# Kernel tuning notes

Hardware: AMD Instinct MI355X
Metric: run time of the kernel (lower is better)

## Reference

```python
import jax, jax.numpy as jnp
import numpy as np

N, E, H, L = 50000, 1_600_000, 128, 3


def _ln(x, g, b, eps=1e-5):
    m = x.mean(-1, keepdims=True)
    v = x.var(-1, keepdims=True)
    return (x - m) / jnp.sqrt(v + eps) * g + b


def _mlp2(inp, w1, b1, g, be, w2, b2):
    # Linear -> LayerNorm -> SiLU -> (Dropout=identity in eval) -> Linear
    h = inp @ w1 + b1
    h = jax.nn.silu(_ln(h, g, be))
    return h @ w2 + b2


def setup_inputs() -> dict:
    key = jax.random.key(0)
    ks = jax.random.split(key, 16)
    s = 0.05
    inp = {
        'x': jax.random.normal(ks[0], (N, 7), jnp.float32),
        'pos': jax.random.normal(ks[1], (N, 3), jnp.float32),
        'edge_index': jax.random.randint(ks[2], (2, E), 0, N, jnp.int64),
        'enc_w1': jax.random.normal(ks[3], (7, H)) * s,
        'enc_b1': jnp.zeros((H,)),
        'enc_g': jnp.ones((H,)),
        'enc_be': jnp.zeros((H,)),
        'enc_w2': jax.random.normal(ks[4], (H, H)) * s,
        'enc_b2': jnp.zeros((H,)),
        'e_w1': jax.random.normal(ks[5], (L, 2 * H + 5, H)) * s,
        'e_b1': jnp.zeros((L, H)),
        'e_g': jnp.ones((L, H)),
        'e_be': jnp.zeros((L, H)),
        'e_w2': jax.random.normal(ks[6], (L, H, H)) * s,
        'e_b2': jnp.zeros((L, H)),
        'n_w1': jax.random.normal(ks[7], (L, 2 * H, H)) * s,
        'n_b1': jnp.zeros((L, H)),
        'n_g': jnp.ones((L, H)),
        'n_be': jnp.zeros((L, H)),
        'n_w2': jax.random.normal(ks[8], (L, H, H)) * s,
        'n_b2': jnp.zeros((L, H)),
        'ln_g': jnp.ones((L, H)),
        'ln_b': jnp.zeros((L, H)),
        'dec_w1': jax.random.normal(ks[9], (H, H)) * s,
        'dec_b1': jnp.zeros((H,)),
        'dec_w2': jax.random.normal(ks[10], (H, H // 2)) * s,
        'dec_b2': jnp.zeros((H // 2,)),
        'dec_w3': jax.random.normal(ks[11], (H // 2, 6)) * s,
        'dec_b3': jnp.zeros((6,)),
    }
    return inp


def reference(x, pos, edge_index, enc_w1, enc_b1, enc_g, enc_be, enc_w2, enc_b2,
              e_w1, e_b1, e_g, e_be, e_w2, e_b2,
              n_w1, n_b1, n_g, n_be, n_w2, n_b2,
              ln_g, ln_b, dec_w1, dec_b1, dec_w2, dec_b2, dec_w3, dec_b3):
    n_nodes = x.shape[0]
    row, col = edge_index[0], edge_index[1]  # row=source(j), col=target(i)

    # physics edge features: [dist, direction(3), 1/r^2]
    diff = pos[col] - pos[row]                          # (E,3)
    dist = jnp.linalg.norm(diff, axis=-1, keepdims=True) + 1e-8
    edge_attr = jnp.concatenate([dist, diff / dist, 1.0 / (dist ** 2 + 1e-6)], -1)

    h = _mlp2(x, enc_w1, enc_b1, enc_g, enc_be, enc_w2, enc_b2)  # (N,H)

    for l in range(L):
        # message: cat(x_i, x_j, edge_attr) -> edge MLP
        msg_in = jnp.concatenate([h[col], h[row], edge_attr], -1)  # (E,2H+5)
        msg = _mlp2(msg_in, e_w1[l], e_b1[l], e_g[l], e_be[l], e_w2[l], e_b2[l])
        # scatter-add aggregate to targets
        aggr = jax.ops.segment_sum(msg, col, num_segments=n_nodes)  # (N,H)
        # update: cat(x, aggr) -> node MLP, then residual + LayerNorm
        h_new = _mlp2(jnp.concatenate([h, aggr], -1),
                      n_w1[l], n_b1[l], n_g[l], n_be[l], n_w2[l], n_b2[l])
        h = _ln(h + h_new, ln_g[l], ln_b[l])

    d = jax.nn.silu(h @ dec_w1 + dec_b1)
    d = jax.nn.silu(d @ dec_w2 + dec_b2)
    delta = d @ dec_w3 + dec_b3                                  # (N,6)
    return x[:, :6] + delta
```

## Files before the change

### kernel.cpp

```cpp
#include <hip/hip_runtime.h>

typedef unsigned short u16;
typedef unsigned int u32;
typedef __bf16 bf16x8 __attribute__((ext_vector_type(8)));
typedef float f32x4 __attribute__((ext_vector_type(4)));
typedef float f32x2 __attribute__((ext_vector_type(2)));

#define AS_STRIDE 136

__device__ __forceinline__ u16 f2bf1(float f) {
  union { __bf16 h; u16 u; } c; c.h = (__bf16)f; return c.u;
}
__device__ __forceinline__ u32 cvt2bf(float a, float b) {
  union { __bf16 h[2]; u32 u; } c; c.h[0] = (__bf16)a; c.h[1] = (__bf16)b; return c.u;
}
__device__ __forceinline__ float bf2f(u16 u) {
  union { u32 u; float f; } v; v.u = ((u32)u) << 16; return v.f;
}
__device__ __forceinline__ float silu_f(float a) {
  return a / (1.f + __expf(-a));
}
__device__ __forceinline__ f32x2 unpk2(u32 p) {
  union { u32 u; float f; } a, b;
  a.u = p << 16; b.u = p & 0xffff0000u;
  return (f32x2){a.f, b.f};
}

__global__ void edge_hist(const int* __restrict__ edst, int E, int* __restrict__ cnt) {
  int i = blockIdx.x * blockDim.x + threadIdx.x;
  if (i < E) atomicAdd(&cnt[edst[i]], 1);
}

__global__ __launch_bounds__(1024)
void scan_kernel(const int* __restrict__ cnt, int* __restrict__ cursor, int Nn) {
  __shared__ int part[1024];
  int t = threadIdx.x;
  int per = (Nn + 1023) / 1024;
  int b = t * per;
  int s = 0;
  for (int i = 0; i < per; i++) { int idx = b + i; if (idx < Nn) s += cnt[idx]; }
  part[t] = s;
  __syncthreads();
  for (int d = 1; d < 1024; d <<= 1) {
    int v = (t >= d) ? part[t - d] : 0;
    __syncthreads();
    part[t] += v;
    __syncthreads();
  }
  int excl = (t == 0) ? 0 : part[t - 1];
  for (int i = 0; i < per; i++) {
    int idx = b + i;
    if (idx < Nn) { cursor[idx] = excl; excl += cnt[idx]; }
  }
}

__global__ void edge_scatter(const int* __restrict__ esrc, const int* __restrict__ edst,
                             int E, int* __restrict__ cursor,
                             int* __restrict__ ssrc, int* __restrict__ sdst) {
  int i = blockIdx.x * blockDim.x + threadIdx.x;
  if (i < E) {
    int d = edst[i];
    int p = atomicAdd(&cursor[d], 1);
    ssrc[p] = esrc[i];
    sdst[p] = d;
  }
}

__global__ void prep_weights(const float* __restrict__ e_w1, const float* __restrict__ e_w2,
                             const float* __restrict__ n_w1, const float* __restrict__ n_w2,
                             u16* __restrict__ eW1T, u16* __restrict__ eW2T,
                             u16* __restrict__ nW1T, u16* __restrict__ nW2T) {
  int i = blockIdx.x * blockDim.x + threadIdx.x;
  const int s1 = 3 * 128 * 256;
  const int s2 = 3 * 128 * 128;
  if (i < s1) {
    int l = i / 32768, r = i % 32768, n = r >> 8, k = r & 255;
    eW1T[i] = f2bf1(e_w1[l * 33408 + k * 128 + n]);
  } else if (i < s1 + s2) {
    int j = i - s1; int l = j / 16384, r = j % 16384, n = r >> 7, k = r & 127;
    eW2T[j] = f2bf1(e_w2[l * 16384 + k * 128 + n]);
  } else if (i < s1 + s2 + s1) {
    int j = i - s1 - s2; int l = j / 32768, r = j % 32768, n = r >> 8, k = r & 255;
    nW1T[j] = f2bf1(n_w1[l * 32768 + k * 128 + n]);
  } else if (i < 2 * s1 + 2 * s2) {
    int j = i - 2 * s1 - s2; int l = j / 16384, r = j % 16384, n = r >> 7, k = r & 127;
    nW2T[j] = f2bf1(n_w2[l * 16384 + k * 128 + n]);
  }
}

__global__ void prep_weights2(const float* __restrict__ enc_w1, const float* __restrict__ enc_w2,
                              const float* __restrict__ dec_w1, const float* __restrict__ dec_w2,
                              const float* __restrict__ dec_w3, const float* __restrict__ e_w1,
                              u16* __restrict__ encW1T, u16* __restrict__ encW2T,
                              u16* __restrict__ decW1T, u16* __restrict__ decW2T,
                              u16* __restrict__ decW3T, u16* __restrict__ eW1cT) {
  int i = blockIdx.x * blockDim.x + threadIdx.x;
  if (i < 4096) {
    int n = i >> 5, k = i & 31;
    encW1T[i] = (k < 7) ? f2bf1(enc_w1[k * 128 + n]) : (u16)0;
  } else if (i < 20480) {
    int j = i - 4096; int n = j >> 7, k = j & 127;
    encW2T[j] = f2bf1(enc_w2[k * 128 + n]);
  } else if (i < 36864) {
    int j = i - 20480; int n = j >> 7, k = j & 127;
    decW1T[j] = f2bf1(dec_w1[k * 128 + n]);
  } else if (i < 45056) {
    int j = i - 36864; int n = j >> 7, k = j & 127;
    decW2T[j] = f2bf1(dec_w2[k * 64 + n]);
  } else if (i < 46080) {
    int j = i - 45056; int n = j >> 6, k = j & 63;
    decW3T[j] = (n < 6) ? f2bf1(dec_w3[k * 6 + n]) : (u16)0;
  } else if (i < 58368) {
    int j = i - 46080; int l = j / 4096, r = j % 4096, n = r >> 5, k = r & 31;
    eW1cT[j] = (k < 5) ? f2bf1(e_w1[l * 33408 + (256 + k) * 128 + n]) : (u16)0;
  }
}

__global__ __launch_bounds__(256, 4)
void encoder_mfma(const float* __restrict__ x,
                  const u16* __restrict__ W1T,
                  const float* __restrict__ b1,
                  const float* __restrict__ g, const float* __restrict__ be,
                  const u16* __restrict__ W2T,
                  const float* __restrict__ b2,
                  const u16* __restrict__ eW1T0,
                  const float* __restrict__ eb10,
                  u16* __restrict__ hbf, u16* __restrict__ hd_all,
                  u16* __restrict__ hs_all, int Nn) {
  __shared__ __align__(16) u16 As[64 * 40];
  __shared__ __align__(16) u16 ts[64 * AS_STRIDE];
  const int tid = threadIdx.x;
  const int m0 = blockIdx.x * 64;
  const int w = tid >> 6, lane = tid & 63, quad = lane >> 4, l16 = lane & 15;
  const int c0w = w * 32;

  if (tid < 64) {
    int node = m0 + tid; if (node >= Nn) node = Nn - 1;
    union { u16 us[32]; uint4 v[4]; } pk;
    #pragma unroll
    for (int k = 0; k < 32; k++) pk.us[k] = 0;
    #pragma unroll
    for (int k = 0; k < 7; k++) pk.us[k] = f2bf1(x[node * 7 + k]);
    #pragma unroll
    for (int k = 0; k < 4; k++) *(uint4*)(As + tid * 40 + k * 8) = pk.v[k];
  }
  __syncthreads();

  f32x4 acc[4][2];
  #pragma unroll
  for (int rt = 0; rt < 4; rt++)
    #pragma unroll
    for (int ct = 0; ct < 2; ct++)
      acc[rt][ct] = (f32x4){0.f, 0.f, 0.f, 0.f};
  {
    const int kl = quad * 8;
    bf16x8 af[4];
    #pragma unroll
    for (int rt = 0; rt < 4; rt++)
      af[rt] = *(const bf16x8*)(As + (rt * 16 + l16) * 40 + kl);
    #pragma unroll
    for (int ct = 0; ct < 2; ct++) {
      bf16x8 bfv = *(const bf16x8*)(W1T + (c0w + ct * 16 + l16) * 32 + kl);
      #pragma unroll
      for (int rt = 0; rt < 4; rt++)
        acc[rt][ct] = __builtin_amdgcn_mfma_f32_16x16x32_bf16(af[rt], bfv, acc[rt][ct], 0, 0, 0);
    }
  }
  #pragma unroll
  for (int ct = 0; ct < 2; ct++) {
    int n = c0w + ct * 16 + l16;
    float b1v = b1[n];
    #pragma unroll
    for (int rt = 0; rt < 4; rt++)
      #pragma unroll
      for (int r = 0; r < 4; r++)
        ts[(rt * 16 + quad * 4 + r) * AS_STRIDE + n] = f2bf1(acc[rt][ct][r] + b1v);
  }
  __syncthreads();

  {
    int row = tid >> 2, sub = tid & 3;
    float s = 0.f, sq = 0.f, vals[32];
    #pragma unroll
    for (int i = 0; i < 32; i++) {
      float v = bf2f(ts[row * AS_STRIDE + sub + i * 4]);
      vals[i] = v; s += v; sq += v * v;
    }
    s += __shfl_xor(s, 1); sq += __shfl_xor(sq, 1);
    s += __shfl_xor(s, 2); sq += __shfl_xor(sq, 2);
    float mean = s * (1.f / 128.f);
    float rstd = rsqrtf(sq * (1.f / 128.f) - mean * mean + 1e-5f);
    #pragma unroll
    for (int i = 0; i < 32; i++) {
      int c = sub + i * 4;
      float a = (vals[i] - mean) * rstd * g[c] + be[c];
      ts[row * AS_STRIDE + c] = f2bf1(silu_f(a));
    }
  }
  __syncthreads();

  f32x4 acc2[4][2];
  #pragma unroll
  for (int rt = 0; rt < 4; rt++)
    #pragma unroll
    for (int ct = 0; ct < 2; ct++)
      acc2[rt][ct] = (f32x4){0.f, 0.f, 0.f, 0.f};
  #pragma unroll
  for (int kk = 0; kk < 4; kk++) {
    const int kl = kk * 32 + quad * 8;
    bf16x8 af[4];
    #pragma unroll
    for (int rt = 0; rt < 4; rt++)
      af[rt] = *(const bf16x8*)(ts + (rt * 16 + l16) * AS_STRIDE + kl);
    #pragma unroll
    for (int ct = 0; ct < 2; ct++) {
      bf16x8 bfv = *(const bf16x8*)(W2T + (size_t)(c0w + ct * 16 + l16) * 128 + kl);
      #pragma unroll
      for (int rt = 0; rt < 4; rt++)
        acc2[rt][ct] = __builtin_amdgcn_mfma_f32_16x16x32_bf16(af[rt], bfv, acc2[rt][ct], 0, 0, 0);
    }
  }
  __syncthreads();
  #pragma unroll
  for (int ct = 0; ct < 2; ct++) {
    int n = c0w + ct * 16 + l16;
    float b2v = b2[n];
    #pragma unroll
    for (int rt = 0; rt < 4; rt++)
      #pragma unroll
      for (int r = 0; r < 4; r++) {
        int m = rt * 16 + quad * 4 + r;
        int node = m0 + m;
        float hv = acc2[rt][ct][r] + b2v;
        u16 hb = f2bf1(hv);
        ts[m * AS_STRIDE + n] = hb;
        if (node < Nn) hbf[(size_t)node * 128 + n] = hb;
      }
  }
  __syncthreads();

  {
    f32x4 ah[4][2];
    #pragma unroll
    for (int rt = 0; rt < 4; rt++)
      #pragma unroll
      for (int ct = 0; ct < 2; ct++)
        ah[rt][ct] = (f32x4){0.f, 0.f, 0.f, 0.f};
    #pragma unroll
    for (int kk = 0; kk < 4; kk++) {
      const int kl = kk * 32 + quad * 8;
      bf16x8 af[4];
      #pragma unroll
      for (int rt = 0; rt < 4; rt++)
        af[rt] = *(const bf16x8*)(ts + (rt * 16 + l16) * AS_STRIDE + kl);
      #pragma unroll
      for (int ct = 0; ct < 2; ct++) {
        bf16x8 bd = *(const bf16x8*)(eW1T0 + (size_t)(c0w + ct * 16 + l16) * 256 + kl);
        #pragma unroll
        for (int rt = 0; rt < 4; rt++)
          ah[rt][ct] = __builtin_amdgcn_mfma_f32_16x16x32_bf16(af[rt], bd, ah[rt][ct], 0, 0, 0);
      }
    }
    #pragma unroll
    for (int ct = 0; ct < 2; ct++) {
      int n = c0w + ct * 16 + l16;
      float b1v = eb10[n];
      #pragma unroll
      for (int rt = 0; rt < 4; rt++)
        #pragma unroll
        for (int r = 0; r < 4; r++) {
          int node = m0 + rt * 16 + quad * 4 + r;
          if (node < Nn) hd_all[(size_t)node * 128 + n] = f2bf1(ah[rt][ct][r] + b1v);
        }
    }
    #pragma unroll
    for (int rt = 0; rt < 4; rt++)
      #pragma unroll
      for (int ct = 0; ct < 2; ct++)
        ah[rt][ct] = (f32x4){0.f, 0.f, 0.f, 0.f};
    #pragma unroll
    for (int kk = 0; kk < 4; kk++) {
      const int kl = kk * 32 + quad * 8;
      bf16x8 af[4];
      #pragma unroll
      for (int rt = 0; rt < 4; rt++)
        af[rt] = *(const bf16x8*)(ts + (rt * 16 + l16) * AS_STRIDE + kl);
      #pragma unroll
      for (int ct = 0; ct < 2; ct++) {
        bf16x8 bs = *(const bf16x8*)(eW1T0 + (size_t)(c0w + ct * 16 + l16) * 256 + 128 + kl);
        #pragma unroll
        for (int rt = 0; rt < 4; rt++)
          ah[rt][ct] = __builtin_amdgcn_mfma_f32_16x16x32_bf16(af[rt], bs, ah[rt][ct], 0, 0, 0);
      }
    }
    #pragma unroll
    for (int ct = 0; ct < 2; ct++) {
      int n = c0w + ct * 16 + l16;
      #pragma unroll
      for (int rt = 0; rt < 4; rt++)
        #pragma unroll
        for (int r = 0; r < 4; r++) {
          int node = m0 + rt * 16 + quad * 4 + r;
          if (node < Nn) hs_all[(size_t)node * 128 + n] = f2bf1(ah[rt][ct][r]);
        }
    }
  }
}

__global__ __launch_bounds__(256, 4)
void edge_mlp_kernel(const int* __restrict__ ssrc, const int* __restrict__ sdst,
                     const float* __restrict__ pos,
                     const u16* __restrict__ hd_all, const u16* __restrict__ hs_all,
                     const u16* __restrict__ w1cT,
                     const float* __restrict__ g, const float* __restrict__ be,
                     const u16* __restrict__ W2T,
                     const float* __restrict__ b2,
                     float* __restrict__ aggr) {
  __shared__ int s_dst[64], s_src[64];
  __shared__ __align__(16) u16 s_eaA[64 * 40];
  __shared__ __align__(16) u16 s_t[64 * AS_STRIDE];
  __shared__ __align__(16) u16 s_msg[128 * 68];

  const int tid = threadIdx.x;
  const int e0 = blockIdx.x * 64;
  const int w = tid >> 6, lane = tid & 63, quad = lane >> 4, l16 = lane & 15;
  const int c0w = w * 32;

  if (tid < 64) {
    int src = ssrc[e0 + tid], dst = sdst[e0 + tid];
    s_src[tid] = src; s_dst[tid] = dst;
    float dx = pos[dst * 3 + 0] - pos[src * 3 + 0];
    float dy = pos[dst * 3 + 1] - pos[src * 3 + 1];
    float dz = pos[dst * 3 + 2] - pos[src * 3 + 2];
    float dist = sqrtf(dx * dx + dy * dy + dz * dz) + 1e-8f;
    float inv = 1.f / dist;
    union { u16 us[40]; uint4 v[5]; } pk;
    #pragma unroll
    for (int k = 0; k < 40; k++) pk.us[k] = 0;
    pk.us[0] = f2bf1(dist);
    pk.us[1] = f2bf1(dx * inv); pk.us[2] = f2bf1(dy * inv); pk.us[3] = f2bf1(dz * inv);
    pk.us[4] = f2bf1(1.f / (dist * dist + 1e-6f));
    #pragma unroll
    for (int k = 0; k < 5; k++) *(uint4*)(s_eaA + tid * 40 + k * 8) = pk.v[k];
  }
  __syncthreads();

  {
    f32x4 ae[4][2];
    #pragma unroll
    for (int rt = 0; rt < 4; rt++)
      #pragma unroll
      for (int ct = 0; ct < 2; ct++)
        ae[rt][ct] = (f32x4){0.f, 0.f, 0.f, 0.f};
    const int kl = quad * 8;
    bf16x8 afe[4];
    #pragma unroll
    for (int rt = 0; rt < 4; rt++)
      afe[rt] = *(const bf16x8*)(s_eaA + (rt * 16 + l16) * 40 + kl);
    #pragma unroll
    for (int ct = 0; ct < 2; ct++) {
      bf16x8 bw = *(const bf16x8*)(w1cT + (c0w + ct * 16 + l16) * 32 + kl);
      #pragma unroll
      for (int rt = 0; rt < 4; rt++)
        ae[rt][ct] = __builtin_amdgcn_mfma_f32_16x16x32_bf16(afe[rt], bw, ae[rt][ct], 0, 0, 0);
    }
    #pragma unroll
    for (int ct = 0; ct < 2; ct++) {
      int n = c0w + ct * 16 + l16;
      #pragma unroll
      for (int rt = 0; rt < 4; rt++)
        #pragma unroll
        for (int r = 0; r < 4; r++)
          s_t[(rt * 16 + quad * 4 + r) * AS_STRIDE + n] = f2bf1(ae[rt][ct][r]);
    }
  }
  __syncthreads();

  {
    const int rg = tid >> 4, cg = tid & 15;
    const int c0 = cg * 8;
    f32x2 g2[4], be2[4];
    {
      f32x4 ga = *(const f32x4*)(g + c0), gb = *(const f32x4*)(g + c0 + 4);
      f32x4 ba = *(const f32x4*)(be + c0), bb = *(const f32x4*)(be + c0 + 4);
      g2[0] = (f32x2){ga[0], ga[1]}; g2[1] = (f32x2){ga[2], ga[3]};
      g2[2] = (f32x2){gb[0], gb[1]}; g2[3] = (f32x2){gb[2], gb[3]};
      be2[0] = (f32x2){ba[0], ba[1]}; be2[1] = (f32x2){ba[2], ba[3]};
      be2[2] = (f32x2){bb[0], bb[1]}; be2[3] = (f32x2){bb[2], bb[3]};
    }
    #pragma unroll
    for (int rr = 0; rr < 4; rr++) {
      int m = rg * 4 + rr;
      int d = s_dst[m], sidx = s_src[m];
      uint4 hd4 = *(const uint4*)(hd_all + (size_t)d * 128 + c0);
      uint4 hs4 = *(const uint4*)(hs_all + (size_t)sidx * 128 + c0);
      uint4 te4 = *(const uint4*)(s_t + m * AS_STRIDE + c0);
      u32 hp[4] = {hd4.x, hd4.y, hd4.z, hd4.w};
      u32 sp[4] = {hs4.x, hs4.y, hs4.z, hs4.w};
      u32 tp[4] = {te4.x, te4.y, te4.z, te4.w};
      f32x2 t2[4], sm2 = (f32x2){0.f, 0.f}, sq2 = (f32x2){0.f, 0.f};
      #pragma unroll
      for (int p = 0; p < 4; p++) {
        t2[p] = unpk2(hp[p]) + unpk2(sp[p]) + unpk2(tp[p]);
        sm2 += t2[p];
        sq2 += t2[p] * t2[p];
      }
      float sm = sm2[0] + sm2[1], sq = sq2[0] + sq2[1];
      sm += __shfl_xor(sm, 1);  sq += __shfl_xor(sq, 1);
      sm += __shfl_xor(sm, 2);  sq += __shfl_xor(sq, 2);
      sm += __shfl_xor(sm, 4);  sq += __shfl_xor(sq, 4);
      sm += __shfl_xor(sm, 8);  sq += __shfl_xor(sq, 8);
      float mean = sm * (1.f / 128.f);
      float rstd = rsqrtf(sq * (1.f / 128.f) - mean * mean + 1e-5f);
      f32x2 sc = (f32x2){rstd, rstd};
      f32x2 ofs = (f32x2){-mean * rstd, -mean * rstd};
      float o[8];
      #pragma unroll
      for (int p = 0; p < 4; p++) {
        f32x2 a = t2[p] * sc + ofs;
        a = a * g2[p] + be2[p];
        o[2 * p]     = silu_f(a[0]);
        o[2 * p + 1] = silu_f(a[1]);
      }
      uint4 st;
      st.x = cvt2bf(o[0], o[1]); st.y = cvt2bf(o[2], o[3]);
      st.z = cvt2bf(o[4], o[5]); st.w = cvt2bf(o[6], o[7]);
      *(uint4*)(s_t + m * AS_STRIDE + c0) = st;
    }
  }
  __syncthreads();

  f32x4 acc2[4][2];
  #pragma unroll
  for (int rt = 0; rt < 4; rt++)
    #pragma unroll
    for (int ct = 0; ct < 2; ct++)
      acc2[rt][ct] = (f32x4){0.f, 0.f, 0.f, 0.f};

  #pragma unroll
  for (int kk = 0; kk < 4; kk++) {
    const int kl = kk * 32 + quad * 8;
    bf16x8 af[4];
    #pragma unroll
    for (int rt = 0; rt < 4; rt++)
      af[rt] = *(const bf16x8*)(s_t + (rt * 16 + l16) * AS_STRIDE + kl);
    #pragma unroll
    for (int ct = 0; ct < 2; ct++) {
      bf16x8 bfv = *(const bf16x8*)(W2T + (size_t)(c0w + ct * 16 + l16) * 128 + kl);
      #pragma unroll
      for (int rt = 0; rt < 4; rt++)
        acc2[rt][ct] = __builtin_amdgcn_mfma_f32_16x16x32_bf16(af[rt], bfv, acc2[rt][ct], 0, 0, 0);
    }
  }

  #pragma unroll
  for (int ct = 0; ct < 2; ct++) {
    int n = c0w + ct * 16 + l16;
    float b2v = b2[n];
    #pragma unroll
    for (int rt = 0; rt < 4; rt++) {
      int mb = rt * 16 + quad * 4;
      uint2 st;
      st.x = cvt2bf(acc2[rt][ct][0] + b2v, acc2[rt][ct][1] + b2v);
      st.y = cvt2bf(acc2[rt][ct][2] + b2v, acc2[rt][ct][3] + b2v);
      *(uint2*)(s_msg + n * 68 + mb) = st;
    }
  }
  __syncthreads();

  {
    int c = tid & 127, q = tid >> 7;
    int r0 = q * 32;
    const u16* mp = s_msg + c * 68 + r0;
    float run = 0.f; int cur = s_dst[r0];
    #pragma unroll
    for (int i = 0; i < 16; i++) {
      u32 pr = *(const u32*)(mp + 2 * i);
      union { u32 u; float f; } a, b;
      a.u = pr << 16; b.u = pr & 0xffff0000u;
      int d0 = s_dst[r0 + 2 * i], d1 = s_dst[r0 + 2 * i + 1];
      if (d0 != cur) { atomicAdd(&aggr[(size_t)cur * 128 + c], run); run = 0.f; cur = d0; }
      run += a.f;
      if (d1 != cur) { atomicAdd(&aggr[(size_t)cur * 128 + c], run); run = 0.f; cur = d1; }
      run += b.f;
    }
    atomicAdd(&aggr[(size_t)cur * 128 + c], run);
  }
}

__global__ __launch_bounds__(256, 4)
void node_mlp_kernel(u16* __restrict__ hbf, const float* __restrict__ aggr,
                     const u16* __restrict__ W1T, const float* __restrict__ b1,
                     const float* __restrict__ g, const float* __restrict__ be,
                     const u16* __restrict__ W2T, const float* __restrict__ b2,
                     const float* __restrict__ lng, const float* __restrict__ lnb,
                     const u16* __restrict__ W1Tn, const float* __restrict__ b1n,
                     u16* __restrict__ hd_all, u16* __restrict__ hs_all,
                     int Nn) {
  __shared__ __align__(16) u16 As[128 * AS_STRIDE];
  u16* t_su = As;
  u16* u_su = As + 64 * AS_STRIDE;

  const int tid = threadIdx.x;
  const int m0 = blockIdx.x * 64;
  const int w = tid >> 6, lane = tid & 63, quad = lane >> 4, l16 = lane & 15;
  const int c0w = w * 32;

  {
    int r = tid >> 4, c8 = (tid & 15) * 8;
    #pragma unroll
    for (int rp = 0; rp < 4; rp++) {
      int m = rp * 16 + r;
      int node = m0 + m; if (node >= Nn) node = Nn - 1;
      *(uint4*)(As + m * AS_STRIDE + c8) = *(const uint4*)(hbf + (size_t)node * 128 + c8);
      const float* ap = aggr + (size_t)node * 128 + c8;
      float4 f0 = *(const float4*)ap;
      float4 f1 = *(const float4*)(ap + 4);
      uint4 pk;
      pk.x = cvt2bf(f0.x, f0.y); pk.y = cvt2bf(f0.z, f0.w);
      pk.z = cvt2bf(f1.x, f1.y); pk.w = cvt2bf(f1.z, f1.w);
      *(uint4*)(As + (64 + m) * AS_STRIDE + c8) = pk;
    }
  }
  __syncthreads();

  f32x4 acc[4][2];
  #pragma unroll
  for (int rt = 0; rt < 4; rt++)
    #pragma unroll
    for (int ct = 0; ct < 2; ct++)
      acc[rt][ct] = (f32x4){0.f, 0.f, 0.f, 0.f};

  #pragma unroll
  for (int kk = 0; kk < 8; kk++) {
    const u16* Ab = As + (kk < 4 ? 0 : 64 * AS_STRIDE);
    const int kl = (kk & 3) * 32 + quad * 8;
    bf16x8 af[4];
    #pragma unroll
    for (int rt = 0; rt < 4; rt++)
      af[rt] = *(const bf16x8*)(Ab + (rt * 16 + l16) * AS_STRIDE + kl);
    const int kg = kk * 32 + quad * 8;
    #pragma unroll
    for (int ct = 0; ct < 2; ct++) {
      bf16x8 bfv = *(const bf16x8*)(W1T + (size_t)(c0w + ct * 16 + l16) * 256 + kg);
      #pragma unroll
      for (int rt = 0; rt < 4; rt++)
        acc[rt][ct] = __builtin_amdgcn_mfma_f32_16x16x32_bf16(af[rt], bfv, acc[rt][ct], 0, 0, 0);
    }
  }

  float b1v[2];
  #pragma unroll
  for (int ct = 0; ct < 2; ct++) b1v[ct] = b1[c0w + ct * 16 + l16];
  __syncthreads();

  #pragma unroll
  for (int rt = 0; rt < 4; rt++)
    #pragma unroll
    for (int ct = 0; ct < 2; ct++) {
      int n = c0w + ct * 16 + l16;
      #pragma unroll
      for (int r = 0; r < 4; r++)
        t_su[(rt * 16 + quad * 4 + r) * AS_STRIDE + n] = f2bf1(acc[rt][ct][r] + b1v[ct]);
    }
  __syncthreads();

  {
    int row = tid >> 2, sub = tid & 3;
    float s = 0.f, sq = 0.f, vals[32];
    #pragma unroll
    for (int i = 0; i < 32; i++) {
      float v = bf2f(t_su[row * AS_STRIDE + sub + i * 4]);
      vals[i] = v; s += v; sq += v * v;
    }
    s += __shfl_xor(s, 1); sq += __shfl_xor(sq, 1);
    s += __shfl_xor(s, 2); sq += __shfl_xor(sq, 2);
    float mean = s * (1.f / 128.f);
    float rstd = rsqrtf(sq * (1.f / 128.f) - mean * mean + 1e-5f);
    #pragma unroll
    for (int i = 0; i < 32; i++) {
      int c = sub + i * 4;
      float a = (vals[i] - mean) * rstd * g[c] + be[c];
      u_su[row * AS_STRIDE + c] = f2bf1(silu_f(a));
    }
  }
  __syncthreads();

  f32x4 acc2[4][2];
  #pragma unroll
  for (int rt = 0; rt < 4; rt++)
    #pragma unroll
    for (int ct = 0; ct < 2; ct++)
      acc2[rt][ct] = (f32x4){0.f, 0.f, 0.f, 0.f};

  #pragma unroll
  for (int kk = 0; kk < 4; kk++) {
    const int kl = kk * 32 + quad * 8;
    bf16x8 af[4];
    #pragma unroll
    for (int rt = 0; rt < 4; rt++)
      af[rt] = *(const bf16x8*)(u_su + (rt * 16 + l16) * AS_STRIDE + kl);
    #pragma unroll
    for (int ct = 0; ct < 2; ct++) {
      bf16x8 bfv = *(const bf16x8*)(W2T + (size_t)(c0w + ct * 16 + l16) * 128 + kl);
      #pragma unroll
      for (int rt = 0; rt < 4; rt++)
        acc2[rt][ct] = __builtin_amdgcn_mfma_f32_16x16x32_bf16(af[rt], bfv, acc2[rt][ct], 0, 0, 0);
    }
  }
  __syncthreads();

  #pragma unroll
  for (int ct = 0; ct < 2; ct++) {
    int n = c0w + ct * 16 + l16;
    float b2v = b2[n];
    #pragma unroll
    for (int rt = 0; rt < 4; rt++)
      #pragma unroll
      for (int r = 0; r < 4; r++) {
        int m = rt * 16 + quad * 4 + r;
        int node = m0 + m; if (node >= Nn) node = Nn - 1;
        t_su[m * AS_STRIDE + n] =
            f2bf1(acc2[rt][ct][r] + b2v + bf2f(hbf[(size_t)node * 128 + n]));
      }
  }
  __syncthreads();

  {
    int row = tid >> 2, sub = tid & 3;
    int node = m0 + row;
    float s = 0.f, sq = 0.f, vals[32];
    #pragma unroll
    for (int i = 0; i < 32; i++) {
      float v = bf2f(t_su[row * AS_STRIDE + sub + i * 4]);
      vals[i] = v; s += v; sq += v * v;
    }
    s += __shfl_xor(s, 1); sq += __shfl_xor(sq, 1);
    s += __shfl_xor(s, 2); sq += __shfl_xor(sq, 2);
    float mean = s * (1.f / 128.f);
    float rstd = rsqrtf(sq * (1.f / 128.f) - mean * mean + 1e-5f);
    #pragma unroll
    for (int i = 0; i < 32; i++) {
      int c = sub + i * 4;
      float v = (vals[i] - mean) * rstd * lng[c] + lnb[c];
      u16 hb = f2bf1(v);
      t_su[row * AS_STRIDE + c] = hb;
      if (node < Nn) hbf[(size_t)node * 128 + c] = hb;
    }
  }

  if (W1Tn != nullptr) {
    __syncthreads();
    f32x4 ah[4][2];
    #pragma unroll
    for (int rt = 0; rt < 4; rt++)
      #pragma unroll
      for (int ct = 0; ct < 2; ct++)
        ah[rt][ct] = (f32x4){0.f, 0.f, 0.f, 0.f};
    #pragma unroll
    for (int kk = 0; kk < 4; kk++) {
      const int kl = kk * 32 + quad * 8;
      bf16x8 af[4];
      #pragma unroll
      for (int rt = 0; rt < 4; rt++)
        af[rt] = *(const bf16x8*)(t_su + (rt * 16 + l16) * AS_STRIDE + kl);
      #pragma unroll
      for (int ct = 0; ct < 2; ct++) {
        bf16x8 bd = *(const bf16x8*)(W1Tn + (size_t)(c0w + ct * 16 + l16) * 256 + kl);
        #pragma unroll
        for (int rt = 0; rt < 4; rt++)
          ah[rt][ct] = __builtin_amdgcn_mfma_f32_16x16x32_bf16(af[rt], bd, ah[rt][ct], 0, 0, 0);
      }
    }
    #pragma unroll
    for (int ct = 0; ct < 2; ct++) {
      int n = c0w + ct * 16 + l16;
      float bv = b1n[n];
      #pragma unroll
      for (int rt = 0; rt < 4; rt++)
        #pragma unroll
        for (int r = 0; r < 4; r++) {
          int node = m0 + rt * 16 + quad * 4 + r;
          if (node < Nn) hd_all[(size_t)node * 128 + n] = f2bf1(ah[rt][ct][r] + bv);
        }
    }
    #pragma unroll
    for (int rt = 0; rt < 4; rt++)
      #pragma unroll
      for (int ct = 0; ct < 2; ct++)
        ah[rt][ct] = (f32x4){0.f, 0.f, 0.f, 0.f};
    #pragma unroll
    for (int kk = 0; kk < 4; kk++) {
      const int kl = kk * 32 + quad * 8;
      bf16x8 af[4];
      #pragma unroll
      for (int rt = 0; rt < 4; rt++)
        af[rt] = *(const bf16x8*)(t_su + (rt * 16 + l16) * AS_STRIDE + kl);
      #pragma unroll
      for (int ct = 0; ct < 2; ct++) {
        bf16x8 bs = *(const bf16x8*)(W1Tn + (size_t)(c0w + ct * 16 + l16) * 256 + 128 + kl);
        #pragma unroll
        for (int rt = 0; rt < 4; rt++)
          ah[rt][ct] = __builtin_amdgcn_mfma_f32_16x16x32_bf16(af[rt], bs, ah[rt][ct], 0, 0, 0);
      }
    }
    #pragma unroll
    for (int ct = 0; ct < 2; ct++) {
      int n = c0w + ct * 16 + l16;
      #pragma unroll
      for (int rt = 0; rt < 4; rt++)
        #pragma unroll
        for (int r = 0; r < 4; r++) {
          int node = m0 + rt * 16 + quad * 4 + r;
          if (node < Nn) hs_all[(size_t)node * 128 + n] = f2bf1(ah[rt][ct][r]);
        }
    }
  }
}

__global__ __launch_bounds__(256, 4)
void decoder_mfma(const float* __restrict__ x, const u16* __restrict__ hbf,
                  const u16* __restrict__ W1T,
                  const float* __restrict__ b1,
                  const u16* __restrict__ W2T,
                  const float* __restrict__ b2,
                  const u16* __restrict__ W3T,
                  const float* __restrict__ b3,
                  float* __restrict__ out, int Nn) {
  __shared__ __align__(16) u16 u1[64 * AS_STRIDE];
  __shared__ __align__(16) u16 u2[64 * 72];
  const int tid = threadIdx.x;
  const int m0 = blockIdx.x * 64;
  const int w = tid >> 6, lane = tid & 63, quad = lane >> 4, l16 = lane & 15;
  const int c0w = w * 32;

  {
    int r = tid >> 4, c8 = (tid & 15) * 8;
    #pragma unroll
    for (int rp = 0; rp < 4; rp++) {
      int m = rp * 16 + r;
      int node = m0 + m; if (node >= Nn) node = Nn - 1;
      *(uint4*)(u1 + m * AS_STRIDE + c8) = *(const uint4*)(hbf + (size_t)node * 128 + c8);
    }
  }
  __syncthreads();

  f32x4 acc[4][2];
  #pragma unroll
  for (int rt = 0; rt < 4; rt++)
    #pragma unroll
    for (int ct = 0; ct < 2; ct++)
      acc[rt][ct] = (f32x4){0.f, 0.f, 0.f, 0.f};
  #pragma unroll
  for (int kk = 0; kk < 4; kk++) {
    const int kl = kk * 32 + quad * 8;
    bf16x8 af[4];
    #pragma unroll
    for (int rt = 0; rt < 4; rt++)
      af[rt] = *(const bf16x8*)(u1 + (rt * 16 + l16) * AS_STRIDE + kl);
    #pragma unroll
    for (int ct = 0; ct < 2; ct++) {
      bf16x8 bfv = *(const bf16x8*)(W1T + (size_t)(c0w + ct * 16 + l16) * 128 + kl);
      #pragma unroll
      for (int rt = 0; rt < 4; rt++)
        acc[rt][ct] = __builtin_amdgcn_mfma_f32_16x16x32_bf16(af[rt], bfv, acc[rt][ct], 0, 0, 0);
    }
  }
  __syncthreads();
  #pragma unroll
  for (int ct = 0; ct < 2; ct++) {
    int n = c0w + ct * 16 + l16;
    float b1v = b1[n];
    #pragma unroll
    for (int rt = 0; rt < 4; rt++)
      #pragma unroll
      for (int r = 0; r < 4; r++)
        u1[(rt * 16 + quad * 4 + r) * AS_STRIDE + n] = f2bf1(silu_f(acc[rt][ct][r] + b1v));
  }
  __syncthreads();

  {
    const int c0b = w * 16;
    f32x4 a2[4];
    #pragma unroll
    for (int rt = 0; rt < 4; rt++) a2[rt] = (f32x4){0.f, 0.f, 0.f, 0.f};
    #pragma unroll
    for (int kk = 0; kk < 4; kk++) {
      const int kl = kk * 32 + quad * 8;
      bf16x8 af[4];
      #pragma unroll
      for (int rt = 0; rt < 4; rt++)
        af[rt] = *(const bf16x8*)(u1 + (rt * 16 + l16) * AS_STRIDE + kl);
      bf16x8 bfv = *(const bf16x8*)(W2T + (size_t)(c0b + l16) * 128 + kl);
      #pragma unroll
      for (int rt = 0; rt < 4; rt++)
        a2[rt] = __builtin_amdgcn_mfma_f32_16x16x32_bf16(af[rt], bfv, a2[rt], 0, 0, 0);
    }
    float b2v = b2[c0b + l16];
    __syncthreads();
    #pragma unroll
    for (int rt = 0; rt < 4; rt++)
      #pragma unroll
      for (int r = 0; r < 4; r++)
        u2[(rt * 16 + quad * 4 + r) * 72 + c0b + l16] = f2bf1(silu_f(a2[rt][r] + b2v));
  }
  __syncthreads();

  if (w == 0) {
    f32x4 a3[4];
    #pragma unroll
    for (int rt = 0; rt < 4; rt++) a3[rt] = (f32x4){0.f, 0.f, 0.f, 0.f};
    #pragma unroll
    for (int kk = 0; kk < 2; kk++) {
      const int kl = kk * 32 + quad * 8;
      bf16x8 af[4];
      #pragma unroll
      for (int rt = 0; rt < 4; rt++)
        af[rt] = *(const bf16x8*)(u2 + (rt * 16 + l16) * 72 + kl);
      bf16x8 bfv = *(const bf16x8*)(W3T + l16 * 64 + kl);
      #pragma unroll
      for (int rt = 0; rt < 4; rt++)
        a3[rt] = __builtin_amdgcn_mfma_f32_16x16x32_bf16(af[rt], bfv, a3[rt], 0, 0, 0);
    }
    if (l16 < 6) {
      float b3v = b3[l16];
      #pragma unroll
      for (int rt = 0; rt < 4; rt++)
        #pragma unroll
        for (int r = 0; r < 4; r++) {
          int node = m0 + rt * 16 + quad * 4 + r;
          if (node < Nn)
            out[(size_t)node * 6 + l16] = a3[rt][r] + b3v + x[node * 7 + l16];
        }
    }
  }
}

extern "C" void kernel_launch(void* const* d_in, const int* in_sizes, int n_in,
                              void* d_out, int out_size, void* d_ws, size_t ws_size,
                              hipStream_t stream) {
  const float* x      = (const float*)d_in[0];
  const float* pos    = (const float*)d_in[1];
  const int*   eidx   = (const int*)d_in[2];
  const float* enc_w1 = (const float*)d_in[3];
  const float* enc_b1 = (const float*)d_in[4];
  const float* enc_g  = (const float*)d_in[5];
  const float* enc_be = (const float*)d_in[6];
  const float* enc_w2 = (const float*)d_in[7];
  const float* enc_b2 = (const float*)d_in[8];
  const float* e_w1   = (const float*)d_in[9];
  const float* e_b1   = (const float*)d_in[10];
  const float* e_g    = (const float*)d_in[11];
  const float* e_be   = (const float*)d_in[12];
  const float* e_w2   = (const float*)d_in[13];
  const float* e_b2   = (const float*)d_in[14];
  const float* n_w1   = (const float*)d_in[15];
  const float* n_b1   = (const float*)d_in[16];
  const float* n_g    = (const float*)d_in[17];
  const float* n_be   = (const float*)d_in[18];
  const float* n_w2   = (const float*)d_in[19];
  const float* n_b2   = (const float*)d_in[20];
  const float* ln_g   = (const float*)d_in[21];
  const float* ln_b   = (const float*)d_in[22];
  const float* dec_w1 = (const float*)d_in[23];
  const float* dec_b1 = (const float*)d_in[24];
  const float* dec_w2 = (const float*)d_in[25];
  const float* dec_b2 = (const float*)d_in[26];
  const float* dec_w3 = (const float*)d_in[27];
  const float* dec_b3 = (const float*)d_in[28];

  const int N = in_sizes[0] / 7;
  const int E = in_sizes[2] / 2;

  char* ws = (char*)d_ws;
  size_t off = 0;
  u16*   hbf    = (u16*)(ws + off);   off += (size_t)N * 128 * 2;
  u16*   hd_all = (u16*)(ws + off);   off += (size_t)N * 128 * 2;
  u16*   hs_all = (u16*)(ws + off);   off += (size_t)N * 128 * 2;
  float* aggr   = (float*)(ws + off); off += (size_t)N * 128 * 4;
  u16* eW1T = (u16*)(ws + off); off += 3 * 128 * 256 * 2;
  u16* eW2T = (u16*)(ws + off); off += 3 * 128 * 128 * 2;
  u16* nW1T = (u16*)(ws + off); off += 3 * 128 * 256 * 2;
  u16* nW2T = (u16*)(ws + off); off += 3 * 128 * 128 * 2;
  u16* encW1T = (u16*)(ws + off); off += 128 * 32 * 2;
  u16* encW2T = (u16*)(ws + off); off += 128 * 128 * 2;
  u16* decW1T = (u16*)(ws + off); off += 128 * 128 * 2;
  u16* decW2T = (u16*)(ws + off); off += 64 * 128 * 2;
  u16* decW3T = (u16*)(ws + off); off += 16 * 64 * 2;
  u16* eW1cT  = (u16*)(ws + off); off += 3 * 128 * 32 * 2;
  int* cnt    = (int*)(ws + off); off += (size_t)N * 4;
  int* cursor = (int*)(ws + off); off += (size_t)N * 4;
  int* ssrc   = (int*)(ws + off); off += (size_t)E * 4;
  int* sdst   = (int*)(ws + off); off += (size_t)E * 4;

  hipMemsetAsync(cnt, 0, (size_t)N * 4, stream);
  edge_hist<<<(E + 255) / 256, 256, 0, stream>>>(eidx + E, E, cnt);
  scan_kernel<<<1, 1024, 0, stream>>>(cnt, cursor, N);
  edge_scatter<<<(E + 255) / 256, 256, 0, stream>>>(eidx, eidx + E, E, cursor, ssrc, sdst);

  prep_weights<<<1152, 256, 0, stream>>>(e_w1, e_w2, n_w1, n_w2, eW1T, eW2T, nW1T, nW2T);
  prep_weights2<<<228, 256, 0, stream>>>(enc_w1, enc_w2, dec_w1, dec_w2, dec_w3, e_w1,
                                         encW1T, encW2T, decW1T, decW2T, decW3T, eW1cT);

  const int nblk = (N + 63) / 64;
  encoder_mfma<<<nblk, 256, 0, stream>>>(x, encW1T, enc_b1, enc_g, enc_be, encW2T, enc_b2,
                                         eW1T, e_b1, hbf, hd_all, hs_all, N);

  for (int l = 0; l < 3; l++) {
    hipMemsetAsync(aggr, 0, (size_t)N * 128 * 4, stream);
    edge_mlp_kernel<<<E / 64, 256, 0, stream>>>(
        ssrc, sdst, pos, hd_all, hs_all,
        eW1cT + (size_t)l * 4096,
        e_g + l * 128, e_be + l * 128,
        eW2T + (size_t)l * 128 * 128, e_b2 + l * 128, aggr);
    const u16* W1Tn = (l < 2) ? (eW1T + (size_t)(l + 1) * 128 * 256) : (const u16*)nullptr;
    node_mlp_kernel<<<nblk, 256, 0, stream>>>(
        hbf, aggr,
        nW1T + (size_t)l * 128 * 256, n_b1 + l * 128, n_g + l * 128, n_be + l * 128,
        nW2T + (size_t)l * 128 * 128, n_b2 + l * 128,
        ln_g + l * 128, ln_b + l * 128,
        W1Tn, e_b1 + ((l + 1) % 3) * 128, hd_all, hs_all, N);
  }

  decoder_mfma<<<nblk, 256, 0, stream>>>(x, hbf, decW1T, dec_b1, decW2T, dec_b2,
                                         decW3T, dec_b3, (float*)d_out, N);
}
```

Before: 1.354 ms.

## Fuse decoder into last node MLP, swizzle edge blocks, batch gather loads

The decoder MLP now runs inside the final node_mlp_kernel launch, taking the LayerNormed h from shared memory. This removes one launch and the re-read of hbf. The edge kernel remaps block IDs to interleave edge chunks across 8 groups, which changes locality and the order of scatter atomics. It also issues all hd/hs gather loads before the LayerNorm loop to increase memory-level parallelism, at the cost of more registers. The fused path assumes t_su holds the final h and adds register and shared-memory pressure to the node kernel.

```diff
diff --git a/kernel.cpp b/kernel.cpp
--- a/kernel.cpp
+++ b/kernel.cpp
@@ -231,8 +231,7 @@
       for (int r = 0; r < 4; r++) {
         int m = rt * 16 + quad * 4 + r;
         int node = m0 + m;
-        float hv = acc2[rt][ct][r] + b2v;
-        u16 hb = f2bf1(hv);
+        u16 hb = f2bf1(acc2[rt][ct][r] + b2v);
         ts[m * AS_STRIDE + n] = hb;
         if (node < Nn) hbf[(size_t)node * 128 + n] = hb;
       }
@@ -322,7 +321,8 @@
   __shared__ __align__(16) u16 s_msg[128 * 68];
 
   const int tid = threadIdx.x;
-  const int e0 = blockIdx.x * 64;
+  const int bid = blockIdx.x;
+  const int e0 = ((bid & 7) * (gridDim.x >> 3) + (bid >> 3)) * 64;
   const int w = tid >> 6, lane = tid & 63, quad = lane >> 4, l16 = lane & 15;
   const int c0w = w * 32;
 
@@ -379,6 +379,13 @@
   {
     const int rg = tid >> 4, cg = tid & 15;
     const int c0 = cg * 8;
+    uint4 hd4[4], hs4[4];
+    #pragma unroll
+    for (int rr = 0; rr < 4; rr++) {
+      int m = rg * 4 + rr;
+      hd4[rr] = *(const uint4*)(hd_all + (size_t)s_dst[m] * 128 + c0);
+      hs4[rr] = *(const uint4*)(hs_all + (size_t)s_src[m] * 128 + c0);
+    }
     f32x2 g2[4], be2[4];
     {
       f32x4 ga = *(const f32x4*)(g + c0), gb = *(const f32x4*)(g + c0 + 4);
@@ -391,12 +398,9 @@
     #pragma unroll
     for (int rr = 0; rr < 4; rr++) {
       int m = rg * 4 + rr;
-      int d = s_dst[m], sidx = s_src[m];
-      uint4 hd4 = *(const uint4*)(hd_all + (size_t)d * 128 + c0);
-      uint4 hs4 = *(const uint4*)(hs_all + (size_t)sidx * 128 + c0);
       uint4 te4 = *(const uint4*)(s_t + m * AS_STRIDE + c0);
-      u32 hp[4] = {hd4.x, hd4.y, hd4.z, hd4.w};
-      u32 sp[4] = {hs4.x, hs4.y, hs4.z, hs4.w};
+      u32 hp[4] = {hd4[rr].x, hd4[rr].y, hd4[rr].z, hd4[rr].w};
+      u32 sp[4] = {hs4[rr].x, hs4[rr].y, hs4[rr].z, hs4[rr].w};
       u32 tp[4] = {te4.x, te4.y, te4.z, te4.w};
       f32x2 t2[4], sm2 = (f32x2){0.f, 0.f}, sq2 = (f32x2){0.f, 0.f};
       #pragma unroll
@@ -496,6 +500,11 @@
                      const float* __restrict__ lng, const float* __restrict__ lnb,
                      const u16* __restrict__ W1Tn, const float* __restrict__ b1n,
                      u16* __restrict__ hd_all, u16* __restrict__ hs_all,
+                     const float* __restrict__ x,
+                     const u16* __restrict__ dW1T, const float* __restrict__ db1,
+                     const u16* __restrict__ dW2T, const float* __restrict__ db2,
+                     const u16* __restrict__ dW3T, const float* __restrict__ db3,
+                     float* __restrict__ out,
                      int Nn) {
   __shared__ __align__(16) u16 As[128 * AS_STRIDE];
   u16* t_su = As;
@@ -716,122 +725,94 @@
         }
     }
   }
-}
-
-__global__ __launch_bounds__(256, 4)
-void decoder_mfma(const float* __restrict__ x, const u16* __restrict__ hbf,
-                  const u16* __restrict__ W1T,
-                  const float* __restrict__ b1,
-                  const u16* __restrict__ W2T,
-                  const float* __restrict__ b2,
-                  const u16* __restrict__ W3T,
-                  const float* __restrict__ b3,
-                  float* __restrict__ out, int Nn) {
-  __shared__ __align__(16) u16 u1[64 * AS_STRIDE];
-  __shared__ __align__(16) u16 u2[64 * 72];
-  const int tid = threadIdx.x;
-  const int m0 = blockIdx.x * 64;
-  const int w = tid >> 6, lane = tid & 63, quad = lane >> 4, l16 = lane & 15;
-  const int c0w = w * 32;
-
-  {
-    int r = tid >> 4, c8 = (tid & 15) * 8;
-    #pragma unroll
-    for (int rp = 0; rp < 4; rp++) {
-      int m = rp * 16 + r;
-      int node = m0 + m; if (node >= Nn) node = Nn - 1;
-      *(uint4*)(u1 + m * AS_STRIDE + c8) = *(const uint4*)(hbf + (size_t)node * 128 + c8);
-    }
-  }
-  __syncthreads();
-
-  f32x4 acc[4][2];
-  #pragma unroll
-  for (int rt = 0; rt < 4; rt++)
-    #pragma unroll
-    for (int ct = 0; ct < 2; ct++)
-      acc[rt][ct] = (f32x4){0.f, 0.f, 0.f, 0.f};
-  #pragma unroll
-  for (int kk = 0; kk < 4; kk++) {
-    const int kl = kk * 32 + quad * 8;
-    bf16x8 af[4];
-    #pragma unroll
-    for (int rt = 0; rt < 4; rt++)
-      af[rt] = *(const bf16x8*)(u1 + (rt * 16 + l16) * AS_STRIDE + kl);
-    #pragma unroll
-    for (int ct = 0; ct < 2; ct++) {
-      bf16x8 bfv = *(const bf16x8*)(W1T + (size_t)(c0w + ct * 16 + l16) * 128 + kl);
-      #pragma unroll
-      for (int rt = 0; rt < 4; rt++)
-        acc[rt][ct] = __builtin_amdgcn_mfma_f32_16x16x32_bf16(af[rt], bfv, acc[rt][ct], 0, 0, 0);
-    }
-  }
-  __syncthreads();
-  #pragma unroll
-  for (int ct = 0; ct < 2; ct++) {
-    int n = c0w + ct * 16 + l16;
-    float b1v = b1[n];
-    #pragma unroll
-    for (int rt = 0; rt < 4; rt++)
-      #pragma unroll
-      for (int r = 0; r < 4; r++)
-        u1[(rt * 16 + quad * 4 + r) * AS_STRIDE + n] = f2bf1(silu_f(acc[rt][ct][r] + b1v));
-  }
-  __syncthreads();
-
-  {
-    const int c0b = w * 16;
-    f32x4 a2[4];
-    #pragma unroll
-    for (int rt = 0; rt < 4; rt++) a2[rt] = (f32x4){0.f, 0.f, 0.f, 0.f};
+
+  if (dW1T != nullptr) {
+    __syncthreads();
+    f32x4 da[4][2];
+    #pragma unroll
+    for (int rt = 0; rt < 4; rt++)
+      #pragma unroll
+      for (int ct = 0; ct < 2; ct++)
+        da[rt][ct] = (f32x4){0.f, 0.f, 0.f, 0.f};
     #pragma unroll
     for (int kk = 0; kk < 4; kk++) {
       const int kl = kk * 32 + quad * 8;
       bf16x8 af[4];
       #pragma unroll
       for (int rt = 0; rt < 4; rt++)
-        af[rt] = *(const bf16x8*)(u1 + (rt * 16 + l16) * AS_STRIDE + kl);
-      bf16x8 bfv = *(const bf16x8*)(W2T + (size_t)(c0b + l16) * 128 + kl);
-      #pragma unroll
-      for (int rt = 0; rt < 4; rt++)
-        a2[rt] = __builtin_amdgcn_mfma_f32_16x16x32_bf16(af[rt], bfv, a2[rt], 0, 0, 0);
-    }
-    float b2v = b2[c0b + l16];
+        af[rt] = *(const bf16x8*)(t_su + (rt * 16 + l16) * AS_STRIDE + kl);
+      #pragma unroll
+      for (int ct = 0; ct < 2; ct++) {
+        bf16x8 bfv = *(const bf16x8*)(dW1T + (size_t)(c0w + ct * 16 + l16) * 128 + kl);
+        #pragma unroll
+        for (int rt = 0; rt < 4; rt++)
+          da[rt][ct] = __builtin_amdgcn_mfma_f32_16x16x32_bf16(af[rt], bfv, da[rt][ct], 0, 0, 0);
+      }
+    }
     __syncthreads();
     #pragma unroll
-    for (int rt = 0; rt < 4; rt++)
-      #pragma unroll
-      for (int r = 0; r < 4; r++)
-        u2[(rt * 16 + quad * 4 + r) * 72 + c0b + l16] = f2bf1(silu_f(a2[rt][r] + b2v));
-  }
-  __syncthreads();
-
-  if (w == 0) {
-    f32x4 a3[4];
-    #pragma unroll
-    for (int rt = 0; rt < 4; rt++) a3[rt] = (f32x4){0.f, 0.f, 0.f, 0.f};
-    #pragma unroll
-    for (int kk = 0; kk < 2; kk++) {
-      const int kl = kk * 32 + quad * 8;
-      bf16x8 af[4];
-      #pragma unroll
-      for (int rt = 0; rt < 4; rt++)
-        af[rt] = *(const bf16x8*)(u2 + (rt * 16 + l16) * 72 + kl);
-      bf16x8 bfv = *(const bf16x8*)(W3T + l16 * 64 + kl);
-      #pragma unroll
-      for (int rt = 0; rt < 4; rt++)
-        a3[rt] = __builtin_amdgcn_mfma_f32_16x16x32_bf16(af[rt], bfv, a3[rt], 0, 0, 0);
-    }
-    if (l16 < 6) {
-      float b3v = b3[l16];
-      #pragma unroll
-      for (int rt = 0; rt < 4; rt++)
-        #pragma unroll
-        for (int r = 0; r < 4; r++) {
-          int node = m0 + rt * 16 + quad * 4 + r;
-          if (node < Nn)
-            out[(size_t)node * 6 + l16] = a3[rt][r] + b3v + x[node * 7 + l16];
-        }
+    for (int ct = 0; ct < 2; ct++) {
+      int n = c0w + ct * 16 + l16;
+      float bv = db1[n];
+      #pragma unroll
+      for (int rt = 0; rt < 4; rt++)
+        #pragma unroll
+        for (int r = 0; r < 4; r++)
+          u_su[(rt * 16 + quad * 4 + r) * AS_STRIDE + n] = f2bf1(silu_f(da[rt][ct][r] + bv));
+    }
+    __syncthreads();
+    {
+      const int c0b = w * 16;
+      f32x4 a2[4];
+      #pragma unroll
+      for (int rt = 0; rt < 4; rt++) a2[rt] = (f32x4){0.f, 0.f, 0.f, 0.f};
+      #pragma unroll
+      for (int kk = 0; kk < 4; kk++) {
+        const int kl = kk * 32 + quad * 8;
+        bf16x8 af[4];
+        #pragma unroll
+        for (int rt = 0; rt < 4; rt++)
+          af[rt] = *(const bf16x8*)(u_su + (rt * 16 + l16) * AS_STRIDE + kl);
+        bf16x8 bfv = *(const bf16x8*)(dW2T + (size_t)(c0b + l16) * 128 + kl);
+        #pragma unroll
+        for (int rt = 0; rt < 4; rt++)
+          a2[rt] = __builtin_amdgcn_mfma_f32_16x16x32_bf16(af[rt], bfv, a2[rt], 0, 0, 0);
+      }
+      float bv = db2[c0b + l16];
+      #pragma unroll
+      for (int rt = 0; rt < 4; rt++)
+        #pragma unroll
+        for (int r = 0; r < 4; r++)
+          t_su[(rt * 16 + quad * 4 + r) * 72 + c0b + l16] = f2bf1(silu_f(a2[rt][r] + bv));
+    }
+    __syncthreads();
+    if (w == 0) {
+      f32x4 a3[4];
+      #pragma unroll
+      for (int rt = 0; rt < 4; rt++) a3[rt] = (f32x4){0.f, 0.f, 0.f, 0.f};
+      #pragma unroll
+      for (int kk = 0; kk < 2; kk++) {
+        const int kl = kk * 32 + quad * 8;
+        bf16x8 af[4];
+        #pragma unroll
+        for (int rt = 0; rt < 4; rt++)
+          af[rt] = *(const bf16x8*)(t_su + (rt * 16 + l16) * 72 + kl);
+        bf16x8 bfv = *(const bf16x8*)(dW3T + l16 * 64 + kl);
+        #pragma unroll
+        for (int rt = 0; rt < 4; rt++)
+          a3[rt] = __builtin_amdgcn_mfma_f32_16x16x32_bf16(af[rt], bfv, a3[rt], 0, 0, 0);
+      }
+      if (l16 < 6) {
+        float bv = db3[l16];
+        #pragma unroll
+        for (int rt = 0; rt < 4; rt++)
+          #pragma unroll
+          for (int r = 0; r < 4; r++) {
+            int node = m0 + rt * 16 + quad * 4 + r;
+            if (node < Nn)
+              out[(size_t)node * 6 + l16] = a3[rt][r] + bv + x[node * 7 + l16];
+          }
+      }
     }
   }
 }
@@ -914,14 +895,17 @@
         e_g + l * 128, e_be + l * 128,
         eW2T + (size_t)l * 128 * 128, e_b2 + l * 128, aggr);
     const u16* W1Tn = (l < 2) ? (eW1T + (size_t)(l + 1) * 128 * 256) : (const u16*)nullptr;
+    const bool last = (l == 2);
     node_mlp_kernel<<<nblk, 256, 0, stream>>>(
         hbf, aggr,
         nW1T + (size_t)l * 128 * 256, n_b1 + l * 128, n_g + l * 128, n_be + l * 128,
         nW2T + (size_t)l * 128 * 128, n_b2 + l * 128,
         ln_g + l * 128, ln_b + l * 128,
-        W1Tn, e_b1 + ((l + 1) % 3) * 128, hd_all, hs_all, N);
-  }
-
-  decoder_mfma<<<nblk, 256, 0, stream>>>(x, hbf, decW1T, dec_b1, decW2T, dec_b2,
-                                         decW3T, dec_b3, (float*)d_out, N);
-}
+        W1Tn, e_b1 + ((l + 1) % 3) * 128, hd_all, hs_all,
+        x,
+        last ? decW1T : (const u16*)nullptr, dec_b1,
+        last ? decW2T : (const u16*)nullptr, dec_b2,
+        last ? decW3T : (const u16*)nullptr, dec_b3,
+        (float*)d_out, N);
+  }
+}
```

Result: no change. 1.360 ms (+0.5%).
